# Performance work log

Measured on AMD Instinct MI355X. Metric: run time of the kernel, lower is better.

Reference implementation:

```python
import jax, jax.numpy as jnp
import numpy as np

EMBD = 256
HEAD = 4
HEAD_DIM = EMBD // HEAD  # 64


def setup_inputs() -> dict:
    key = jax.random.key(0)
    ks = jax.random.split(key, 5)
    B, S = 16, 1024
    scale = 1.0 / np.sqrt(EMBD)
    return {
        "x": jax.random.normal(ks[0], (B, S, EMBD), dtype=jnp.float32),
        "W_qkv": jax.random.normal(ks[1], (EMBD, 3 * EMBD), dtype=jnp.float32) * scale,
        "b_qkv": jax.random.normal(ks[2], (3 * EMBD,), dtype=jnp.float32) * 0.01,
        "W_out": jax.random.normal(ks[3], (EMBD, EMBD), dtype=jnp.float32) * scale,
        "b_out": jax.random.normal(ks[4], (EMBD,), dtype=jnp.float32) * 0.01,
    }


def reference(x, W_qkv, b_qkv, W_out, b_out):
    B, S, E = x.shape
    qkv = x @ W_qkv + b_qkv  # [B,S,3E]
    q, k, v = jnp.split(qkv, 3, axis=-1)
    # [B,S,E] -> [B,H,S,D]
    q = q.reshape(B, S, HEAD, HEAD_DIM).transpose(0, 2, 1, 3)
    k = k.reshape(B, S, HEAD, HEAD_DIM).transpose(0, 2, 1, 3)
    v = v.reshape(B, S, HEAD, HEAD_DIM).transpose(0, 2, 1, 3)
    att = jnp.einsum("bhqd,bhkd->bhqk", q, k) / jnp.sqrt(jnp.float32(HEAD_DIM))
    causal = jnp.tril(jnp.ones((S, S), dtype=bool))
    att = jnp.where(causal, att, -jnp.inf)
    att = jax.nn.softmax(att, axis=-1)
    out = jnp.einsum("bhqk,bhkd->bhqd", att, v)  # [B,H,S,D]
    out = out.transpose(0, 2, 1, 3).reshape(B, S, E)
    return out @ W_out + b_out
```

## Files before the change

### kernel.cpp

```cpp
#include <hip/hip_runtime.h>


typedef unsigned short ushort_t;
typedef __bf16 bf16x8 __attribute__((ext_vector_type(8)));
typedef unsigned short u16x8 __attribute__((ext_vector_type(8)));
typedef float f32x4 __attribute__((ext_vector_type(4)));

__device__ __forceinline__ ushort_t f2bf(float f) {
  unsigned u = __builtin_bit_cast(unsigned, f);
  u += 0x7fffu + ((u >> 16) & 1u);
  return (ushort_t)(u >> 16);
}

__device__ __forceinline__ void gload_lds16(const ushort_t* g, ushort_t* l) {
  __builtin_amdgcn_global_load_lds(
      (const __attribute__((address_space(1))) unsigned int*)g,
      (__attribute__((address_space(3))) unsigned int*)l, 16, 0, 0);
}

#define BARRIER_RAW() do { __builtin_amdgcn_s_barrier(); \
                           __builtin_amdgcn_sched_barrier(0); } while (0)

__global__ __launch_bounds__(256)
void convert_all(const float* __restrict__ x,
                 const float* __restrict__ Wq, const float* __restrict__ Wo,
                 ushort_t* __restrict__ xb,
                 ushort_t* __restrict__ WqT, ushort_t* __restrict__ WoT)
{
  int blk = blockIdx.x;
  if (blk < 2048) {
    const size_t base = (size_t)blk * 2048 + threadIdx.x * 8;
    float4 v0 = *(const float4*)&x[base];
    float4 v1 = *(const float4*)&x[base + 4];
    u16x8 ov;
    ov[0]=f2bf(v0.x); ov[1]=f2bf(v0.y); ov[2]=f2bf(v0.z); ov[3]=f2bf(v0.w);
    ov[4]=f2bf(v1.x); ov[5]=f2bf(v1.y); ov[6]=f2bf(v1.z); ov[7]=f2bf(v1.w);
    *(u16x8*)&xb[base] = ov;
    return;
  }
  blk -= 2048;
  __shared__ float t[64][65];
  const float* src; ushort_t* dst; int ld_src, k0, n0;
  if (blk < 48) { src = Wq; dst = WqT; ld_src = 768;
                  k0 = (blk / 12) * 64; n0 = (blk % 12) * 64; }
  else { blk -= 48; src = Wo; dst = WoT; ld_src = 256;
         k0 = (blk / 4) * 64; n0 = (blk % 4) * 64; }
  const int tr = threadIdx.x >> 6, tc = threadIdx.x & 63;
  #pragma unroll
  for (int i = 0; i < 16; ++i) {
    const int r = i * 4 + tr;
    t[r][tc] = src[(size_t)(k0 + r) * ld_src + n0 + tc];
  }
  __syncthreads();
  #pragma unroll
  for (int i = 0; i < 16; ++i) {
    const int r = i * 4 + tr;
    dst[(size_t)(n0 + r) * 256 + k0 + tc] = f2bf(t[tc][r]);
  }
}

template<int OUT_MODE, int NB>
__global__ __launch_bounds__(256, 2)
void gemm_bias(const ushort_t* __restrict__ A, int ldA,
               const ushort_t* __restrict__ Bt,
               const float* __restrict__ bias,
               void* __restrict__ Outp, int ldOut,
               ushort_t* __restrict__ Vt)
{
  __shared__ ushort_t Bl[64][256];
  __shared__ ushort_t Al[3][128][32];

  const int tid = threadIdx.x;
  const int lane = tid & 63;
  const int w  = tid >> 6;
  const int wm = w >> 1, wn = w & 1;
  const int l15 = lane & 15, g = lane >> 4;

  const int chunkXCD = (NB * 64) >> 3;
  const int gidx = (blockIdx.x & 7) * chunkXCD + (blockIdx.x >> 3);
  const int mg = gidx / NB;
  const int n0 = (gidx % NB) * 64;
  const int mBase = mg * 256;
  const bool vmode = (OUT_MODE == 0) && (n0 >= 512);

  #pragma unroll
  for (int i = 0; i < 8; ++i) {
    const int L = i * 256 + tid;
    const int r = L >> 5, c = L & 31;
    gload_lds16(&Bt[(size_t)(n0 + r) * 256 + (c ^ (r & 7)) * 8],
                &Bl[0][0] + (size_t)L * 8);
  }
  #pragma unroll
  for (int s = 0; s < 2; ++s) {
    #pragma unroll
    for (int i = 0; i < 2; ++i) {
      const int L = i * 256 + tid;
      const int r = L >> 2, c = L & 3;
      gload_lds16(&A[(size_t)(mBase + r) * ldA + s*32 + (c ^ ((r>>1)&3)) * 8],
                  &Al[s][0][0] + (size_t)L * 8);
    }
  }
  asm volatile("s_waitcnt vmcnt(2)" ::: "memory");
  BARRIER_RAW();

  f32x4 acc[2][4][2] = {};

  #pragma unroll
  for (int t = 0; t < 16; ++t) {
    {
      const int st = (t + 2 < 16) ? t + 2 : 15;
      const int smt = st >> 3, skt = st & 7;
      #pragma unroll
      for (int i = 0; i < 2; ++i) {
        const int L = i * 256 + tid;
        const int r = L >> 2, c = L & 3;
        gload_lds16(&A[(size_t)(mBase + smt*128 + r) * ldA + skt*32
                       + (c ^ ((r>>1)&3)) * 8],
                    &Al[(t + 2) % 3][0][0] + (size_t)L * 8);
      }
    }
    {
      const int mt = t >> 3, kt = t & 7;
      bf16x8 af[4], bfr[2];
      #pragma unroll
      for (int mi = 0; mi < 4; ++mi) {
        const int row = wm*64 + mi*16 + l15;
        af[mi] = __builtin_bit_cast(bf16x8,
            *(const u16x8*)&Al[t % 3][row][(g ^ ((row>>1)&3)) * 8]);
      }
      #pragma unroll
      for (int ni = 0; ni < 2; ++ni) {
        const int row = wn*32 + ni*16 + l15;
        const int c = kt*4 + g;
        bfr[ni] = __builtin_bit_cast(bf16x8,
            *(const u16x8*)&Bl[row][(c ^ (row & 7)) * 8]);
      }
      if (vmode) {
        #pragma unroll
        for (int mi = 0; mi < 4; ++mi)
          #pragma unroll
          for (int ni = 0; ni < 2; ++ni)
            acc[mt][mi][ni] = __builtin_amdgcn_mfma_f32_16x16x32_bf16(
                                  bfr[ni], af[mi], acc[mt][mi][ni], 0, 0, 0);
      } else {
        #pragma unroll
        for (int mi = 0; mi < 4; ++mi)
          #pragma unroll
          for (int ni = 0; ni < 2; ++ni)
            acc[mt][mi][ni] = __builtin_amdgcn_mfma_f32_16x16x32_bf16(
                                  af[mi], bfr[ni], acc[mt][mi][ni], 0, 0, 0);
      }
    }
    asm volatile("s_waitcnt vmcnt(2)" ::: "memory");
    BARRIER_RAW();
  }

  #pragma unroll
  for (int mt = 0; mt < 2; ++mt)
    #pragma unroll
    for (int mi = 0; mi < 4; ++mi)
      #pragma unroll
      for (int ni = 0; ni < 2; ++ni) {
        if (!vmode) {
          const int col = n0 + wn*32 + ni*16 + l15;
          const float bv = bias[col];
          #pragma unroll
          for (int r = 0; r < 4; ++r) {
            const int row = mBase + mt*128 + wm*64 + mi*16 + g*4 + r;
            const float v = acc[mt][mi][ni][r] + bv;
            if (OUT_MODE == 1)
              ((float*)Outp)[(size_t)row * ldOut + col] = v;
            else
              ((ushort_t*)Outp)[(size_t)row * 512 + col] = f2bf(v);
          }
        } else {
          const int hh = (n0 - 512) >> 6;
          const int m = mBase + mt*128 + wm*64 + mi*16 + l15;
          const int bb = m >> 10, ss = m & 1023;
          ushort_t* vbase =
              &Vt[(size_t)(((bb*4 + hh)*16 + (ss >> 6)) * 4096) + (ss & 63)];
          #pragma unroll
          for (int r = 0; r < 4; ++r) {
            const int nn = n0 + wn*32 + ni*16 + g*4 + r;
            const float v = acc[mt][mi][ni][r] + bias[nn];
            vbase[(size_t)((nn - 512) & 63) * 64] = f2bf(v);
          }
        }
      }
}

__global__ __launch_bounds__(256, 2)
void attn_kernel(ushort_t* __restrict__ qk, const ushort_t* __restrict__ Vt)
{
  __shared__ ushort_t K_lds[3][64][64];
  __shared__ ushort_t V_lds[3][64][64];
  __shared__ ushort_t P_lds[4][16][72];

  const int lid = blockIdx.x;
  const int p   = (lid >> 3) & 7;
  const int bh  = (lid & 7) + ((lid >> 6) << 3);
  const int h = bh & 3, b = bh >> 2;
  const int qtA = p, qtB = 15 - p;

  const int tid = threadIdx.x;
  const int lane = tid & 63;
  const int w = tid >> 6;
  const int l15 = lane & 15, g = lane >> 4;

  const size_t rowbase = (size_t)b * 1024;
  const int qc = h * 64, kc = 256 + h * 64;
  const ushort_t* Vtt = Vt + (size_t)bh * 16 * 4096;

  bf16x8 qfA[2], qfB[2];
  {
    const size_t ra = rowbase + qtA*64 + w*16 + l15;
    const size_t rb = rowbase + qtB*64 + w*16 + l15;
    #pragma unroll
    for (int ks = 0; ks < 2; ++ks) {
      qfA[ks] = __builtin_bit_cast(bf16x8,
                  *(const u16x8*)&qk[ra*512 + qc + ks*32 + g*8]);
      qfB[ks] = __builtin_bit_cast(bf16x8,
                  *(const u16x8*)&qk[rb*512 + qc + ks*32 + g*8]);
    }
  }

  f32x4 oA[4] = {}, oB[4] = {};
  float lsA[4] = {0.f,0.f,0.f,0.f}, lsB[4] = {0.f,0.f,0.f,0.f};
  const int qrA0 = qtA*64 + w*16 + g*4;
  const int qrB0 = qtB*64 + w*16 + g*4;

  auto stage = [&](int bi, int kt) {
    const int kv0 = kt * 64;
    const ushort_t* vtile = Vtt + kt * 4096;
    #pragma unroll
    for (int ri = 0; ri < 2; ++ri) {
      const int L = ri*256 + tid;
      const int r = L >> 3;
      const int c = (L & 7) ^ (r & 7);
      gload_lds16(&qk[(rowbase + kv0 + r)*512 + kc + c*8],
                  &K_lds[bi][0][0] + (size_t)L*8);
      gload_lds16(&vtile[r*64 + c*8],
                  &V_lds[bi][0][0] + (size_t)L*8);
    }
  };

  stage(0, 0);
  stage(1, 1);
  asm volatile("s_waitcnt vmcnt(4)" ::: "memory");
  BARRIER_RAW();

  for (int kt = 0; kt <= qtB; ++kt) {
    const int cur = kt % 3;
    stage((kt + 2) % 3, (kt + 2 <= qtB) ? kt + 2 : qtB);

    bf16x8 kf[2][4], vf[2][4];
    #pragma unroll
    for (int ks = 0; ks < 2; ++ks)
      #pragma unroll
      for (int ni = 0; ni < 4; ++ni) {
        const int row = ni*16 + l15;
        const int cc  = (((ks*4 + g) ^ (row & 7))) * 8;
        kf[ks][ni] = __builtin_bit_cast(bf16x8, *(const u16x8*)&K_lds[cur][row][cc]);
        vf[ks][ni] = __builtin_bit_cast(bf16x8, *(const u16x8*)&V_lds[cur][row][cc]);
      }

    const int kv0 = kt * 64;

    auto tile_step = [&](const bf16x8 (&qf)[2], f32x4 (&o)[4], float (&ls)[4],
                         int qr0, bool diag) {
      f32x4 s[4] = {};
      #pragma unroll
      for (int ks = 0; ks < 2; ++ks)
        #pragma unroll
        for (int ni = 0; ni < 4; ++ni)
          s[ni] = __builtin_amdgcn_mfma_f32_16x16x32_bf16(qf[ks], kf[ks][ni],
                                                          s[ni], 0, 0, 0);
      #pragma unroll
      for (int r = 0; r < 4; ++r)
        #pragma unroll
        for (int ni = 0; ni < 4; ++ni) {
          float e = __expf(fmaf(s[ni][r], 0.125f, -10.0f));
          if (diag) e = (kv0 + ni*16 + l15 <= qr0 + r) ? e : 0.0f;
          ls[r] += e;
          P_lds[w][g*4 + r][ni*16 + l15] = __builtin_bit_cast(ushort_t, (__bf16)e);
        }
      #pragma unroll
      for (int ks = 0; ks < 2; ++ks) {
        bf16x8 pf = __builtin_bit_cast(bf16x8,
                      *(const u16x8*)&P_lds[w][l15][ks*32 + g*8]);
        #pragma unroll
        for (int di = 0; di < 4; ++di)
          o[di] = __builtin_amdgcn_mfma_f32_16x16x32_bf16(pf, vf[ks][di],
                                                          o[di], 0, 0, 0);
      }
    };

    tile_step(qfB, oB, lsB, qrB0, kt == qtB);
    if (kt <= qtA) tile_step(qfA, oA, lsA, qrA0, kt == qtA);

    asm volatile("s_waitcnt vmcnt(4)" ::: "memory");
    BARRIER_RAW();
  }

  #pragma unroll
  for (int r = 0; r < 4; ++r) {
    #pragma unroll
    for (int d = 1; d < 16; d <<= 1) {
      lsA[r] += __shfl_xor(lsA[r], d);
      lsB[r] += __shfl_xor(lsB[r], d);
    }
  }

  #pragma unroll
  for (int r = 0; r < 4; ++r) {
    const float invA = 1.f / lsA[r];
    const float invB = 1.f / lsB[r];
    const size_t rowA = rowbase + qtA*64 + w*16 + g*4 + r;
    const size_t rowB = rowbase + qtB*64 + w*16 + g*4 + r;
    #pragma unroll
    for (int di = 0; di < 4; ++di) {
      qk[rowA*512 + qc + di*16 + l15] = f2bf(oA[di][r] * invA);
      qk[rowB*512 + qc + di*16 + l15] = f2bf(oB[di][r] * invB);
    }
  }
}

extern "C" void kernel_launch(void* const* d_in, const int* in_sizes, int n_in,
                              void* d_out, int out_size, void* d_ws, size_t ws_size,
                              hipStream_t stream)
{
  const float* x     = (const float*)d_in[0];
  const float* W_qkv = (const float*)d_in[1];
  const float* b_qkv = (const float*)d_in[2];
  const float* W_out = (const float*)d_in[3];
  const float* b_out = (const float*)d_in[4];
  float* out = (float*)d_out;

  char* ws = (char*)d_ws;
  ushort_t* WqT = (ushort_t*)ws;
  ushort_t* WoT = (ushort_t*)(ws + 393216);
  ushort_t* qk  = (ushort_t*)(ws + 524288);
  ushort_t* Vt  = (ushort_t*)(ws + 17301504);
  ushort_t* xb  = (ushort_t*)(ws + 25690112);

  convert_all<<<dim3(2112), dim3(256), 0, stream>>>(x, W_qkv, W_out, xb, WqT, WoT);
  gemm_bias<0, 12><<<dim3(768), dim3(256), 0, stream>>>(
      xb, 256, WqT, b_qkv, qk, 512, Vt);
  attn_kernel<<<dim3(512), dim3(256), 0, stream>>>(qk, Vt);
  gemm_bias<1, 4><<<dim3(256), dim3(256), 0, stream>>>(
      qk, 512, WoT, b_out, out, 256, nullptr);
}
```

Baseline: 67.26 us.

## Compute transposed scores so P stays in registers, removing LDS round-trip

The QK^T MFMA now runs with operands swapped, so each lane holds the scores of a single query row across key positions. Those values feed the PV product directly as B operands of a 16x16x16 bf16 MFMA, which removes the P_lds write/read round-trip and its LDS traffic. The V tile swizzle changes to match the new 4-element fragment reads, the row-sum reduction shrinks to two shuffles, and the output is written as 4-wide vector stores. In exchange it issues twice as many smaller MFMAs for PV, and the added s_nop stalls and the hand-written MFMA fallback could hurt or be fragile.

Measured after the change: 66.13 us. Within noise of the previous version (-1.7%).

```diff
diff --git a/kernel.cpp b/kernel.cpp
--- a/kernel.cpp
+++ b/kernel.cpp
@@ -3,8 +3,11 @@
 
 typedef unsigned short ushort_t;
 typedef __bf16 bf16x8 __attribute__((ext_vector_type(8)));
+typedef __bf16 bf16x4 __attribute__((ext_vector_type(4)));
 typedef unsigned short u16x8 __attribute__((ext_vector_type(8)));
+typedef unsigned short u16x4 __attribute__((ext_vector_type(4)));
 typedef float f32x4 __attribute__((ext_vector_type(4)));
+typedef short s16x4 __attribute__((ext_vector_type(4)));
 
 __device__ __forceinline__ ushort_t f2bf(float f) {
   unsigned u = __builtin_bit_cast(unsigned, f);
@@ -20,6 +23,20 @@
 
 #define BARRIER_RAW() do { __builtin_amdgcn_s_barrier(); \
                            __builtin_amdgcn_sched_barrier(0); } while (0)
+
+__device__ __forceinline__ f32x4 mfma16(bf16x4 a, bf16x4 b, f32x4 c) {
+#if __has_builtin(__builtin_amdgcn_mfma_f32_16x16x16bf16_1k)
+  return __builtin_amdgcn_mfma_f32_16x16x16bf16_1k(
+      __builtin_bit_cast(s16x4, a), __builtin_bit_cast(s16x4, b), c, 0, 0, 0);
+#elif __has_builtin(__builtin_amdgcn_mfma_f32_16x16x16_bf16)
+  return __builtin_amdgcn_mfma_f32_16x16x16_bf16(a, b, c, 0, 0, 0);
+#else
+  f32x4 d = c;
+  asm volatile("v_mfma_f32_16x16x16_bf16 %0, %1, %2, %0"
+               : "+v"(d) : "v"(a), "v"(b));
+  return d;
+#endif
+}
 
 __global__ __launch_bounds__(256)
 void convert_all(const float* __restrict__ x,
@@ -194,7 +211,6 @@
 {
   __shared__ ushort_t K_lds[3][64][64];
   __shared__ ushort_t V_lds[3][64][64];
-  __shared__ ushort_t P_lds[4][16][72];
 
   const int lid = blockIdx.x;
   const int p   = (lid >> 3) & 7;
@@ -225,9 +241,9 @@
   }
 
   f32x4 oA[4] = {}, oB[4] = {};
-  float lsA[4] = {0.f,0.f,0.f,0.f}, lsB[4] = {0.f,0.f,0.f,0.f};
-  const int qrA0 = qtA*64 + w*16 + g*4;
-  const int qrB0 = qtB*64 + w*16 + g*4;
+  float lsA = 0.f, lsB = 0.f;
+  const int qgA = qtA*64 + w*16 + l15;
+  const int qgB = qtB*64 + w*16 + l15;
 
   auto stage = [&](int bi, int kt) {
     const int kv0 = kt * 64;
@@ -236,10 +252,9 @@
     for (int ri = 0; ri < 2; ++ri) {
       const int L = ri*256 + tid;
       const int r = L >> 3;
-      const int c = (L & 7) ^ (r & 7);
-      gload_lds16(&qk[(rowbase + kv0 + r)*512 + kc + c*8],
+      gload_lds16(&qk[(rowbase + kv0 + r)*512 + kc + ((L & 7) ^ (r & 7))*8],
                   &K_lds[bi][0][0] + (size_t)L*8);
-      gload_lds16(&vtile[r*64 + c*8],
+      gload_lds16(&vtile[r*64 + ((L & 7) ^ ((r >> 1) & 7))*8],
                   &V_lds[bi][0][0] + (size_t)L*8);
     }
   };
@@ -253,74 +268,82 @@
     const int cur = kt % 3;
     stage((kt + 2) % 3, (kt + 2 <= qtB) ? kt + 2 : qtB);
 
-    bf16x8 kf[2][4], vf[2][4];
+    bf16x8 kf[2][4];
     #pragma unroll
     for (int ks = 0; ks < 2; ++ks)
       #pragma unroll
       for (int ni = 0; ni < 4; ++ni) {
         const int row = ni*16 + l15;
-        const int cc  = (((ks*4 + g) ^ (row & 7))) * 8;
-        kf[ks][ni] = __builtin_bit_cast(bf16x8, *(const u16x8*)&K_lds[cur][row][cc]);
-        vf[ks][ni] = __builtin_bit_cast(bf16x8, *(const u16x8*)&V_lds[cur][row][cc]);
+        kf[ks][ni] = __builtin_bit_cast(bf16x8,
+            *(const u16x8*)&K_lds[cur][row][(((ks*4 + g) ^ (row & 7))) * 8]);
+      }
+    bf16x4 vf[4][4];
+    #pragma unroll
+    for (int ni = 0; ni < 4; ++ni)
+      #pragma unroll
+      for (int da = 0; da < 4; ++da) {
+        const int row = da*16 + l15;
+        const int phys = (ni*2 + (g >> 1)) ^ ((row >> 1) & 7);
+        vf[ni][da] = __builtin_bit_cast(bf16x4,
+            *(const u16x4*)&V_lds[cur][row][phys*8 + (g & 1)*4]);
       }
 
     const int kv0 = kt * 64;
-
-    auto tile_step = [&](const bf16x8 (&qf)[2], f32x4 (&o)[4], float (&ls)[4],
-                         int qr0, bool diag) {
+    const int g4 = g * 4;
+
+    auto tile_step = [&](const bf16x8 (&qf)[2], f32x4 (&o)[4], float &ls,
+                         int qg, bool diag) {
       f32x4 s[4] = {};
       #pragma unroll
       for (int ks = 0; ks < 2; ++ks)
         #pragma unroll
         for (int ni = 0; ni < 4; ++ni)
-          s[ni] = __builtin_amdgcn_mfma_f32_16x16x32_bf16(qf[ks], kf[ks][ni],
+          s[ni] = __builtin_amdgcn_mfma_f32_16x16x32_bf16(kf[ks][ni], qf[ks],
                                                           s[ni], 0, 0, 0);
-      #pragma unroll
-      for (int r = 0; r < 4; ++r)
-        #pragma unroll
-        for (int ni = 0; ni < 4; ++ni) {
+      bf16x4 pn[4];
+      #pragma unroll
+      for (int ni = 0; ni < 4; ++ni)
+        #pragma unroll
+        for (int r = 0; r < 4; ++r) {
           float e = __expf(fmaf(s[ni][r], 0.125f, -10.0f));
-          if (diag) e = (kv0 + ni*16 + l15 <= qr0 + r) ? e : 0.0f;
-          ls[r] += e;
-          P_lds[w][g*4 + r][ni*16 + l15] = __builtin_bit_cast(ushort_t, (__bf16)e);
+          if (diag) e = (kv0 + ni*16 + g4 + r <= qg) ? e : 0.0f;
+          ls += e;
+          pn[ni][r] = (__bf16)e;
         }
       #pragma unroll
-      for (int ks = 0; ks < 2; ++ks) {
-        bf16x8 pf = __builtin_bit_cast(bf16x8,
-                      *(const u16x8*)&P_lds[w][l15][ks*32 + g*8]);
-        #pragma unroll
-        for (int di = 0; di < 4; ++di)
-          o[di] = __builtin_amdgcn_mfma_f32_16x16x32_bf16(pf, vf[ks][di],
-                                                          o[di], 0, 0, 0);
-      }
+      for (int ni = 0; ni < 4; ++ni)
+        #pragma unroll
+        for (int da = 0; da < 4; ++da)
+          o[da] = mfma16(vf[ni][da], pn[ni], o[da]);
     };
 
-    tile_step(qfB, oB, lsB, qrB0, kt == qtB);
-    if (kt <= qtA) tile_step(qfA, oA, lsA, qrA0, kt == qtA);
+    tile_step(qfB, oB, lsB, qgB, kt == qtB);
+    if (kt <= qtA) tile_step(qfA, oA, lsA, qgA, kt == qtA);
 
     asm volatile("s_waitcnt vmcnt(4)" ::: "memory");
     BARRIER_RAW();
   }
 
-  #pragma unroll
-  for (int r = 0; r < 4; ++r) {
-    #pragma unroll
-    for (int d = 1; d < 16; d <<= 1) {
-      lsA[r] += __shfl_xor(lsA[r], d);
-      lsB[r] += __shfl_xor(lsB[r], d);
-    }
-  }
-
-  #pragma unroll
-  for (int r = 0; r < 4; ++r) {
-    const float invA = 1.f / lsA[r];
-    const float invB = 1.f / lsB[r];
-    const size_t rowA = rowbase + qtA*64 + w*16 + g*4 + r;
-    const size_t rowB = rowbase + qtB*64 + w*16 + g*4 + r;
-    #pragma unroll
-    for (int di = 0; di < 4; ++di) {
-      qk[rowA*512 + qc + di*16 + l15] = f2bf(oA[di][r] * invA);
-      qk[rowB*512 + qc + di*16 + l15] = f2bf(oB[di][r] * invB);
+  asm volatile("s_nop 7\n\ts_nop 7" :::);
+
+  lsA += __shfl_xor(lsA, 16); lsA += __shfl_xor(lsA, 32);
+  lsB += __shfl_xor(lsB, 16); lsB += __shfl_xor(lsB, 32);
+  const float invA = 1.f / lsA;
+  const float invB = 1.f / lsB;
+
+  {
+    const size_t rowA = rowbase + (size_t)qgA;
+    const size_t rowB = rowbase + (size_t)qgB;
+    #pragma unroll
+    for (int da = 0; da < 4; ++da) {
+      u16x4 ovA, ovB;
+      #pragma unroll
+      for (int r = 0; r < 4; ++r) {
+        ovA[r] = f2bf(oA[da][r] * invA);
+        ovB[r] = f2bf(oB[da][r] * invB);
+      }
+      *(u16x4*)&qk[rowA*512 + qc + da*16 + g*4] = ovA;
+      *(u16x4*)&qk[rowB*512 + qc + da*16 + g*4] = ovB;
     }
   }
 }
```
